# Kernel tuning notes

Measured on AMD Instinct MI355X. Metric: run time of the kernel, lower is better.

The kernel has to match this reference:

```python
import jax, jax.numpy as jnp
import numpy as np

RES = 256      # cubic grid resolution
CH = 16        # feature channels
RR = 8         # reduced_res = ceil(log2(RES))
MASK = 128     # low-frequency mask size
N_PTS = 262144 # query points


def _bilinear(feat, gx, gy):
    """torch.F.grid_sample, bilinear, align_corners=True, zero padding.
    feat: (C,H,W); gx,gy: (N,) in [-1,1] (gx indexes W, gy indexes H).
    Returns (N,C)."""
    H, W = feat.shape[1], feat.shape[2]
    x = (gx + 1.0) * 0.5 * (W - 1)
    y = (gy + 1.0) * 0.5 * (H - 1)
    x0 = jnp.floor(x)
    y0 = jnp.floor(y)
    wx = x - x0
    wy = y - y0
    x0i = jnp.clip(x0.astype(jnp.int32), 0, W - 1)
    x1i = jnp.clip(x0i + 1, 0, W - 1)
    y0i = jnp.clip(y0.astype(jnp.int32), 0, H - 1)
    y1i = jnp.clip(y0i + 1, 0, H - 1)
    v00 = feat[:, y0i, x0i]
    v01 = feat[:, y0i, x1i]
    v10 = feat[:, y1i, x0i]
    v11 = feat[:, y1i, x1i]
    out = (v00 * (1 - wx) * (1 - wy) + v01 * wx * (1 - wy)
           + v10 * (1 - wx) * wy + v11 * wx * wy)  # (C,N)
    return out.T


def _plane(P, mask2d, gx, gy, icoord):
    """One phasor plane: mask -> ifft2 -> grid_sample -> Fourier integration.
    P: (CH*RR, RES, RES, 2); returns (N, CH)."""
    Pc = (P[..., 0] + 1j * P[..., 1]) * mask2d          # (C,H,W) complex
    Pc = jnp.fft.ifft2(Pc)                              # ifft over last 2 axes
    C = P.shape[0]
    # interleave (real, imag) per complex channel, like permute+reshape in torch
    feat = jnp.stack([Pc.real, Pc.imag], axis=1).reshape(2 * C, RES, RES)
    samp = _bilinear(feat, gx, gy).reshape(-1, 2 * CH, RR)  # (N, 2*CH, RR)
    Z = samp[:, :CH] + 1j * samp[:, CH:]                    # (N, CH, RR)
    s = (icoord + 1.0) * 0.5 * (2 ** RR - 1)                # scaled coord
    coef = 2.0 ** jnp.arange(RR) - 1.0                      # (RR,)
    basis = jnp.exp(2j * jnp.pi * s[:, None] * coef / (2 ** RR))  # (N, RR)
    return jnp.einsum('nr,ncr->nc', basis, Z).real


def _forward(Pu, Pv, Pw, inputs):
    mask2d = jnp.zeros((RES, RES), jnp.float32).at[:MASK, :MASK].set(1.0)
    out = (_plane(Pu, mask2d, inputs[:, 1], inputs[:, 2], inputs[:, 0])
           + _plane(Pv, mask2d, inputs[:, 0], inputs[:, 2], inputs[:, 1])
           + _plane(Pw, mask2d, inputs[:, 0], inputs[:, 1], inputs[:, 2]))
    return out  # (N, CH)


def setup_inputs() -> dict:
    key = jax.random.key(0)
    k1, k2, k3, k4 = jax.random.split(key, 4)
    Pu = 0.001 * jax.random.normal(k1, (CH * RR, RES, RES, 2), jnp.float32)
    Pv = 0.001 * jax.random.normal(k2, (CH * RR, RES, RES, 2), jnp.float32)
    Pw = 0.001 * jax.random.normal(k3, (CH * RR, RES, RES, 2), jnp.float32)
    inputs = jax.random.uniform(k4, (N_PTS, 3), jnp.float32, -1.0, 1.0)
    return {"Pu": Pu, "Pv": Pv, "Pw": Pw, "inputs": inputs}


def reference(Pu, Pv, Pw, inputs):
    return _forward(Pu, Pv, Pw, inputs)
```

## Files before the change

### kernel.cpp

```cpp
#include <hip/hip_runtime.h>
#include <hip/hip_bf16.h>
#include <hip/hip_fp16.h>
#include <cmath>


#define NPTS 262144

typedef _Float16 f16x2 __attribute__((ext_vector_type(2)));

__device__ __forceinline__ int brev8(int x) { return (int)(__brev((unsigned)x) >> 24); }

__device__ __forceinline__ int swz(int i) {
    return (i & ~15) | ((i ^ (i >> 4)) & 15);
}

__device__ __forceinline__ unsigned pack_bf16(float2 v) {
    unsigned short a = __builtin_bit_cast(unsigned short, __float2bfloat16(v.x));
    unsigned short b = __builtin_bit_cast(unsigned short, __float2bfloat16(v.y));
    return (unsigned)a | ((unsigned)b << 16);
}
__device__ __forceinline__ float2 unpack_bf16(unsigned u) {
    return make_float2(__uint_as_float(u << 16), __uint_as_float(u & 0xffff0000u));
}

__device__ __forceinline__ float dot2f(unsigned a, unsigned b, float c) {
#if __has_builtin(__builtin_amdgcn_fdot2)
    return __builtin_amdgcn_fdot2(__builtin_bit_cast(f16x2, a),
                                  __builtin_bit_cast(f16x2, b), c, false);
#else
    float d;
    asm("v_dot2_f32_f16 %0, %1, %2, %3" : "=v"(d) : "v"(a), "v"(b), "v"(c));
    return d;
#endif
}

__device__ __forceinline__ void plane_coords(int p, float in0, float in1, float in2,
                                             float& gx, float& gy, float& sc) {
    gx = (p == 0) ? in1 : in0;
    gy = (p == 2) ? in1 : in2;
    sc = (p == 0) ? in0 : ((p == 1) ? in1 : in2);
}

__global__ __launch_bounds__(512) void pass1_kernel(const float* __restrict__ P0,
                                                    const float* __restrict__ P1,
                                                    const float* __restrict__ P2,
                                                    unsigned* __restrict__ X) {
    __shared__ float2 tw[128];
    __shared__ float2 tile[256 * 17];

    int t = threadIdx.x;
    if (t < 128) {
        float s, c;
        sincospif((float)t * (1.0f / 128.0f), &s, &c);
        tw[swz(t)] = make_float2(c, s);
    }
    int plane = blockIdx.y;
    const float* P = (plane == 0) ? P0 : ((plane == 1) ? P1 : P2);
    unsigned* Xp = X + (size_t)plane * 4194304;

    int b  = blockIdx.x;
    int ch = b >> 3;
    int x0 = (b & 7) << 4;
    const float* src = P + (size_t)ch * 131072 + x0 * 2;

    const float scale = 1.0f / 65536.0f;
#pragma unroll
    for (int k = 0; k < 2; k++) {
        int i = t + (k << 9);
        int y = i >> 3;
        int j = i & 7;
        float4 v = *(const float4*)(src + (size_t)y * 512 + (j << 2));
        float2 c0 = make_float2(v.x * scale, v.y * scale);
        float2 c1 = make_float2(v.z * scale, v.w * scale);
        int pos = brev8(y);
        tile[swz(pos) * 17 + 2 * j]           = c0;
        tile[swz(pos + 1) * 17 + 2 * j]       = c0;
        tile[swz(pos) * 17 + 2 * j + 1]       = c1;
        tile[swz(pos + 1) * 17 + 2 * j + 1]   = c1;
    }
    __syncthreads();

    int w = t >> 6, l = t & 63;
    int col = (w << 1) + (l & 1);
    int bb  = l >> 1;
#pragma unroll
    for (int s = 2; s <= 8; s++) {
        int half = 1 << (s - 1);
#pragma unroll
        for (int k = 0; k < 4; k++) {
            int bf = (s == 4) ? ((bb << 2) + k) : (bb + (k << 5));
            int j  = bf & (half - 1);
            int g  = bf >> (s - 1);
            int i0 = (g << s) + j;
            int i1 = i0 + half;
            float2 u = tile[swz(i0) * 17 + col];
            float2 v = tile[swz(i1) * 17 + col];
            float2 wq = tw[swz(j << (8 - s))];
            float2 vt = make_float2(v.x * wq.x - v.y * wq.y, v.x * wq.y + v.y * wq.x);
            tile[swz(i0) * 17 + col] = make_float2(u.x + vt.x, u.y + vt.y);
            tile[swz(i1) * 17 + col] = make_float2(u.x - vt.x, u.y - vt.y);
        }
    }
    __syncthreads();

    unsigned* dst = Xp + (size_t)ch * 32768 + x0;
#pragma unroll
    for (int k = 0; k < 8; k++) {
        int i = t + (k << 9);
        int v = i >> 4;
        int c = i & 15;
        dst[(size_t)v * 128 + c] = pack_bf16(tile[swz(v) * 17 + c]);
    }
}

__global__ __launch_bounds__(1024) void pass2_kernel(const unsigned* __restrict__ X,
                                                     __half* __restrict__ feat) {
    __shared__ float2 tw[128];
    __shared__ float2 rows[16 * 257];

    int t = threadIdx.x;
    if (t < 128) {
        float s, c;
        sincospif((float)t * (1.0f / 128.0f), &s, &c);
        tw[swz(t)] = make_float2(c, s);
    }
    int w = t >> 6;
    int l = t & 63;
    int v   = blockIdx.x & 255;
    int g   = blockIdx.x >> 8;
    int ch0 = g << 4;
    int ch  = ch0 + w;
    int plane = blockIdx.y;
    const unsigned* Xp = X + (size_t)plane * 4194304;
    __half* fp = feat + (size_t)plane * 16777216;

    const uint2* src = (const uint2*)(Xp + ((size_t)ch * 256 + v) * 128);
    uint2 d = src[l];
    float2 c0 = unpack_bf16(d.x);
    float2 c1 = unpack_bf16(d.y);
    float2* row = rows + w * 257;
    int p0 = brev8(2 * l);
    int p1 = brev8(2 * l + 1);
    row[swz(p0)]     = c0;
    row[swz(p0 + 1)] = c0;
    row[swz(p1)]     = c1;
    row[swz(p1 + 1)] = c1;
    __syncthreads();
#pragma unroll
    for (int s = 2; s <= 8; s++) {
        int half = 1 << (s - 1);
#pragma unroll
        for (int k = 0; k < 2; k++) {
            int bf = (s == 4) ? ((l << 1) + k) : (l + (k << 6));
            int j  = bf & (half - 1);
            int gg = bf >> (s - 1);
            int i0 = (gg << s) + j;
            int i1 = i0 + half;
            float2 u  = row[swz(i0)];
            float2 vv = row[swz(i1)];
            float2 wq = tw[swz(j << (8 - s))];
            float2 vt = make_float2(vv.x * wq.x - vv.y * wq.y,
                                    vv.x * wq.y + vv.y * wq.x);
            row[swz(i0)] = make_float2(u.x + vt.x, u.y + vt.y);
            row[swz(i1)] = make_float2(u.x - vt.x, u.y - vt.y);
        }
    }
    __syncthreads();
    __half* dst = fp + (size_t)v * 65536 + (ch0 << 1);
#pragma unroll
    for (int k = 0; k < 8; k++) {
        int f = t + (k << 10);
        int x = f >> 5;
        int j = f & 31;
        float2 cpx = rows[(j >> 1) * 257 + swz(x)];
        float val = (j & 1) ? cpx.y : cpx.x;
        dst[x * 256 + j] = __float2half(val * 16384.0f);
    }
}

__device__ __forceinline__ int tile_key(float gx, float gy) {
    float xf = (gx + 1.0f) * 127.5f;
    float yf = (gy + 1.0f) * 127.5f;
    int x0 = max(0, min((int)floorf(xf), 255));
    int y0 = max(0, min((int)floorf(yf), 255));
    return (y0 & 0xF0) | (x0 >> 4);
}

__global__ __launch_bounds__(1024) void hist_kernel(const float* __restrict__ pts,
                                                    unsigned* __restrict__ hist) {
    __shared__ unsigned hb[256];
    int t = threadIdx.x;
    int p = blockIdx.y;
    int n = (blockIdx.x << 10) + t;
    if (t < 256) hb[t] = 0;
    __syncthreads();
    float in0 = pts[3 * n + 0], in1 = pts[3 * n + 1], in2 = pts[3 * n + 2];
    float gx, gy, sc;
    plane_coords(p, in0, in1, in2, gx, gy, sc);
    atomicAdd(&hb[tile_key(gx, gy)], 1u);
    __syncthreads();
    if (t < 256 && hb[t]) atomicAdd(&hist[(p << 8) + t], hb[t]);
}

__global__ __launch_bounds__(256) void scan_kernel(const unsigned* __restrict__ hist,
                                                   unsigned* __restrict__ cursor) {
    __shared__ unsigned s[256];
    int t = threadIdx.x;
    for (int p = 0; p < 3; p++) {
        unsigned v = hist[(p << 8) + t];
        s[t] = v;
        __syncthreads();
#pragma unroll
        for (int d = 1; d < 256; d <<= 1) {
            unsigned add = (t >= d) ? s[t - d] : 0u;
            __syncthreads();
            s[t] += add;
            __syncthreads();
        }
        cursor[(p << 8) + t] = s[t] - v;
        __syncthreads();
    }
}

__global__ __launch_bounds__(1024) void scatter_kernel(const float* __restrict__ pts,
                                                       unsigned* __restrict__ cursor,
                                                       float4* __restrict__ psort) {
    __shared__ unsigned cnt[256];
    __shared__ unsigned base[256];
    int t = threadIdx.x;
    int p = blockIdx.y;
    int n = (blockIdx.x << 10) + t;
    if (t < 256) cnt[t] = 0;
    __syncthreads();
    float in0 = pts[3 * n + 0], in1 = pts[3 * n + 1], in2 = pts[3 * n + 2];
    float gx, gy, sc;
    plane_coords(p, in0, in1, in2, gx, gy, sc);

    float xf = (gx + 1.0f) * 127.5f;
    float yf = (gy + 1.0f) * 127.5f;
    float x0f = floorf(xf);
    float y0f = floorf(yf);
    float wx = xf - x0f;
    float wy = yf - y0f;
    int x0 = max(0, min((int)x0f, 255));
    int y0 = max(0, min((int)y0f, 255));
    int key = (y0 & 0xF0) | (x0 >> 4);

    unsigned rank = atomicAdd(&cnt[key], 1u);
    __syncthreads();
    if (t < 256 && cnt[t]) base[t] = atomicAdd(&cursor[(p << 8) + t], cnt[t]);
    __syncthreads();

    unsigned pk = ((unsigned)((y0 << 8) + x0) << 8)
                | ((x0 < 255) ? (1u << 24) : 0u)
                | ((y0 < 255) ? (1u << 25) : 0u);
    float sprime = (sc + 1.0f) * 0.99609375f;
    __half2 wh = __floats2half2_rn(wx, wy);
    psort[p * NPTS + base[key] + rank] =
        make_float4(__uint_as_float(pk), __builtin_bit_cast(float, wh),
                    sprime, __int_as_float(n));
}


#define GSTAGE(i)                                                              \
    unsigned pk##i = __float_as_uint(pt##i.x);                                 \
    const ushort* bp##i = fb + (pk##i & 0xFFFFFFu);                            \
    int dx##i = (int)((pk##i >> 16) & 0x100u);                                 \
    int dy##i = (int)((pk##i >> 9) & 0x10000u);                                \
    uint4 e00##i = *(const uint4*)(bp##i);                                     \
    uint4 e01##i = *(const uint4*)(bp##i + dx##i);                             \
    uint4 e10##i = *(const uint4*)(bp##i + dy##i);                             \
    uint4 e11##i = *(const uint4*)(bp##i + dx##i + dy##i);

#define GWORK(i) {                                                             \
    __half2 wh = __builtin_bit_cast(__half2, pt##i.y);                         \
    float wx = __low2float(wh);                                                \
    float wy = __high2float(wh);                                               \
    float a = pt##i.z * coef;                                                  \
    float sn, cs;                                                              \
    sincospif(a, &sn, &cs);                                                    \
    float merged = (q < 16) ? cs : -sn;                                        \
    float partner = __int_as_float(                                            \
        __builtin_amdgcn_ds_swizzle(__float_as_int(merged), 0x041F));          \
    float lo = (l & 1) ? partner : merged;                                     \
    float hi = (l & 1) ? merged : partner;                                     \
    __half2 wp = __floats2half2_rn(lo, hi);                                    \
    unsigned wpi = __builtin_bit_cast(unsigned, wp);                           \
    unsigned w0 = (unsigned)__builtin_amdgcn_ds_swizzle((int)wpi, 0x0010);     \
    unsigned w1 = (unsigned)__builtin_amdgcn_ds_swizzle((int)wpi, 0x0050);     \
    unsigned w2 = (unsigned)__builtin_amdgcn_ds_swizzle((int)wpi, 0x0090);     \
    unsigned w3 = (unsigned)__builtin_amdgcn_ds_swizzle((int)wpi, 0x00D0);     \
    float s00 = dot2f(e00##i.w, w3, dot2f(e00##i.z, w2,                        \
                dot2f(e00##i.y, w1, dot2f(e00##i.x, w0, 0.0f))));              \
    float s01 = dot2f(e01##i.w, w3, dot2f(e01##i.z, w2,                        \
                dot2f(e01##i.y, w1, dot2f(e01##i.x, w0, 0.0f))));              \
    float s10 = dot2f(e10##i.w, w3, dot2f(e10##i.z, w2,                        \
                dot2f(e10##i.y, w1, dot2f(e10##i.x, w0, 0.0f))));              \
    float s11 = dot2f(e11##i.w, w3, dot2f(e11##i.z, w2,                        \
                dot2f(e11##i.y, w1, dot2f(e11##i.x, w0, 0.0f))));              \
    const float INV = 6.103515625e-05f;                                        \
    float wys = wy * INV;                                                      \
    float wyc = INV - wys;                                                     \
    float wxc = 1.0f - wx;                                                     \
    float acc = s00 * (wxc * wyc);                                             \
    acc = fmaf(s01, wx * wyc, acc);                                            \
    acc = fmaf(s10, wxc * wys, acc);                                           \
    acc = fmaf(s11, wx * wys, acc);                                            \
    acc += __int_as_float(                                                     \
        __builtin_amdgcn_ds_swizzle(__float_as_int(acc), 0x401F));             \
    if (q < 16) {                                                              \
        int n = __float_as_int(pt##i.w);                                       \
        atomicAdd(&out[((size_t)n << 4) + q], acc);                            \
    } }

__global__ __launch_bounds__(256) void gather_kernel(const ushort* __restrict__ feat,
                                                     const float4* __restrict__ psort,
                                                     float* __restrict__ out) {
    int t = threadIdx.x;
    int w = t >> 6;
    int l = t & 63;
    int h = l >> 5;
    int q = l & 31;
    int p = blockIdx.y;
    const ushort* fb = feat + (size_t)p * 16777216 + (q << 3);

    int b  = blockIdx.x;
    int lb = ((b & 7) << 10) | (b >> 3);
    const float4* ps = psort + p * NPTS + (lb << 5) + (w << 1) + h;

    float4 pt0 = ps[0];
    float4 pt1 = ps[8];
    float4 pt2 = ps[16];
    float4 pt3 = ps[24];

    float coef = (float)((1 << (q & 7)) - 1);

    GSTAGE(0)
    GSTAGE(1)
    GWORK(0)
    GSTAGE(2)
    GWORK(1)
    GSTAGE(3)
    GWORK(2)
    GWORK(3)
}

__global__ __launch_bounds__(256) void combine_kernel(const float4* __restrict__ pa,
                                                      float4* __restrict__ out) {
    int i = (blockIdx.x << 8) + threadIdx.x;
    float4 a = pa[i];
    float4 b = pa[i + 1048576];
    float4 c = pa[i + 2097152];
    out[i] = make_float4(a.x + b.x + c.x, a.y + b.y + c.y,
                         a.z + b.z + c.z, a.w + b.w + c.w);
}

extern "C" void kernel_launch(void* const* d_in, const int* in_sizes, int n_in,
                              void* d_out, int out_size, void* d_ws, size_t ws_size,
                              hipStream_t stream) {
    const float* P0  = (const float*)d_in[0];
    const float* P1  = (const float*)d_in[1];
    const float* P2  = (const float*)d_in[2];
    const float* pts = (const float*)d_in[3];
    float* out = (float*)d_out;
    char* ws = (char*)d_ws;

    __half*   feat   = (__half*)ws;
    unsigned* X      = (unsigned*)(ws + 100663296u);
    float4*   psort  = (float4*)(ws + 201326592u);
    unsigned* hist   = (unsigned*)(ws + 213909504u);
    unsigned* cursor = (unsigned*)(ws + 213912576u);

    hipMemsetAsync(hist, 0, 3072, stream);
    hipMemsetAsync(out, 0, (size_t)NPTS * 64, stream);

    dim3 g1(1024, 3);
    pass1_kernel<<<g1, 512, 0, stream>>>(P0, P1, P2, X);
    dim3 g2(2048, 3);
    pass2_kernel<<<g2, 1024, 0, stream>>>(X, feat);

    dim3 gs(256, 3);
    hist_kernel<<<gs, 1024, 0, stream>>>(pts, hist);
    scan_kernel<<<1, 256, 0, stream>>>(hist, cursor);
    scatter_kernel<<<gs, 1024, 0, stream>>>(pts, cursor, psort);

    dim3 gg(8192, 3);
    gather_kernel<<<gg, 256, 0, stream>>>((const ushort*)feat, psort, out);
}
```

Baseline: 346.8 us.

## Precompute Fourier basis weights in scatter pass and split scan per plane

The scatter kernel now computes the eight cos/sin basis terms per point with one sincospi and angle-doubling recurrences, packs them as fp16 and writes them to a new per-point weight buffer. The gather kernel loads these 32-byte weights instead of evaluating sincospi per lane and shuffling the results across lanes with swizzles. The scan kernel is also split into three blocks, one per plane. The trade is extra global traffic (about 25 MB written and read) and some recurrence rounding error, in exchange for less transcendental and cross-lane work in the gather.

```diff
diff --git a/kernel.cpp b/kernel.cpp
--- a/kernel.cpp
+++ b/kernel.cpp
@@ -21,6 +21,10 @@
 }
 __device__ __forceinline__ float2 unpack_bf16(unsigned u) {
     return make_float2(__uint_as_float(u << 16), __uint_as_float(u & 0xffff0000u));
+}
+__device__ __forceinline__ unsigned pack_h2(float a, float b) {
+    __half2 h = __floats2half2_rn(a, b);
+    return __builtin_bit_cast(unsigned, h);
 }
 
 __device__ __forceinline__ float dot2f(unsigned a, unsigned b, float c) {
@@ -206,25 +210,24 @@
                                                    unsigned* __restrict__ cursor) {
     __shared__ unsigned s[256];
     int t = threadIdx.x;
-    for (int p = 0; p < 3; p++) {
-        unsigned v = hist[(p << 8) + t];
-        s[t] = v;
+    int p = blockIdx.y;
+    unsigned v = hist[(p << 8) + t];
+    s[t] = v;
+    __syncthreads();
+#pragma unroll
+    for (int d = 1; d < 256; d <<= 1) {
+        unsigned add = (t >= d) ? s[t - d] : 0u;
         __syncthreads();
-#pragma unroll
-        for (int d = 1; d < 256; d <<= 1) {
-            unsigned add = (t >= d) ? s[t - d] : 0u;
-            __syncthreads();
-            s[t] += add;
-            __syncthreads();
-        }
-        cursor[(p << 8) + t] = s[t] - v;
+        s[t] += add;
         __syncthreads();
     }
+    cursor[(p << 8) + t] = s[t] - v;
 }
 
 __global__ __launch_bounds__(1024) void scatter_kernel(const float* __restrict__ pts,
                                                        unsigned* __restrict__ cursor,
-                                                       float4* __restrict__ psort) {
+                                                       float4* __restrict__ psort,
+                                                       uint4* __restrict__ pweight) {
     __shared__ unsigned cnt[256];
     __shared__ unsigned base[256];
     int t = threadIdx.x;
@@ -254,11 +257,34 @@
     unsigned pk = ((unsigned)((y0 << 8) + x0) << 8)
                 | ((x0 < 255) ? (1u << 24) : 0u)
                 | ((y0 < 255) ? (1u << 25) : 0u);
-    float sprime = (sc + 1.0f) * 0.99609375f;
+    float sp = (sc + 1.0f) * 0.99609375f;
     __half2 wh = __floats2half2_rn(wx, wy);
-    psort[p * NPTS + base[key] + rank] =
+    int o = base[key] + rank;
+    psort[p * NPTS + o] =
         make_float4(__uint_as_float(pk), __builtin_bit_cast(float, wh),
-                    sprime, __int_as_float(n));
+                    0.0f, __int_as_float(n));
+
+    float c1, s1;
+    sincospif(sp, &s1, &c1);
+    float cc = c1, ss = s1;
+    float cA[8], sA[8];
+    cA[0] = 1.0f; sA[0] = 0.0f;
+    cA[1] = c1;  sA[1] = s1;
+#pragma unroll
+    for (int r = 2; r < 8; r++) {
+        float c2 = cc * cc - ss * ss;
+        float s2 = 2.0f * cc * ss;
+        cc = c2 * c1 - s2 * s1;
+        ss = c2 * s1 + s2 * c1;
+        cA[r] = cc; sA[r] = ss;
+    }
+    uint4 cb = make_uint4(pack_h2(cA[0], cA[1]), pack_h2(cA[2], cA[3]),
+                          pack_h2(cA[4], cA[5]), pack_h2(cA[6], cA[7]));
+    uint4 sb = make_uint4(pack_h2(-sA[0], -sA[1]), pack_h2(-sA[2], -sA[3]),
+                          pack_h2(-sA[4], -sA[5]), pack_h2(-sA[6], -sA[7]));
+    size_t wo = ((size_t)p * NPTS + o) << 1;
+    pweight[wo]     = cb;
+    pweight[wo + 1] = sb;
 }
 
 
@@ -276,28 +302,14 @@
     __half2 wh = __builtin_bit_cast(__half2, pt##i.y);                         \
     float wx = __low2float(wh);                                                \
     float wy = __high2float(wh);                                               \
-    float a = pt##i.z * coef;                                                  \
-    float sn, cs;                                                              \
-    sincospif(a, &sn, &cs);                                                    \
-    float merged = (q < 16) ? cs : -sn;                                        \
-    float partner = __int_as_float(                                            \
-        __builtin_amdgcn_ds_swizzle(__float_as_int(merged), 0x041F));          \
-    float lo = (l & 1) ? partner : merged;                                     \
-    float hi = (l & 1) ? merged : partner;                                     \
-    __half2 wp = __floats2half2_rn(lo, hi);                                    \
-    unsigned wpi = __builtin_bit_cast(unsigned, wp);                           \
-    unsigned w0 = (unsigned)__builtin_amdgcn_ds_swizzle((int)wpi, 0x0010);     \
-    unsigned w1 = (unsigned)__builtin_amdgcn_ds_swizzle((int)wpi, 0x0050);     \
-    unsigned w2 = (unsigned)__builtin_amdgcn_ds_swizzle((int)wpi, 0x0090);     \
-    unsigned w3 = (unsigned)__builtin_amdgcn_ds_swizzle((int)wpi, 0x00D0);     \
-    float s00 = dot2f(e00##i.w, w3, dot2f(e00##i.z, w2,                        \
-                dot2f(e00##i.y, w1, dot2f(e00##i.x, w0, 0.0f))));              \
-    float s01 = dot2f(e01##i.w, w3, dot2f(e01##i.z, w2,                        \
-                dot2f(e01##i.y, w1, dot2f(e01##i.x, w0, 0.0f))));              \
-    float s10 = dot2f(e10##i.w, w3, dot2f(e10##i.z, w2,                        \
-                dot2f(e10##i.y, w1, dot2f(e10##i.x, w0, 0.0f))));              \
-    float s11 = dot2f(e11##i.w, w3, dot2f(e11##i.z, w2,                        \
-                dot2f(e11##i.y, w1, dot2f(e11##i.x, w0, 0.0f))));              \
+    float s00 = dot2f(e00##i.w, ww##i.w, dot2f(e00##i.z, ww##i.z,              \
+                dot2f(e00##i.y, ww##i.y, dot2f(e00##i.x, ww##i.x, 0.0f))));    \
+    float s01 = dot2f(e01##i.w, ww##i.w, dot2f(e01##i.z, ww##i.z,              \
+                dot2f(e01##i.y, ww##i.y, dot2f(e01##i.x, ww##i.x, 0.0f))));    \
+    float s10 = dot2f(e10##i.w, ww##i.w, dot2f(e10##i.z, ww##i.z,              \
+                dot2f(e10##i.y, ww##i.y, dot2f(e10##i.x, ww##i.x, 0.0f))));    \
+    float s11 = dot2f(e11##i.w, ww##i.w, dot2f(e11##i.z, ww##i.z,              \
+                dot2f(e11##i.y, ww##i.y, dot2f(e11##i.x, ww##i.x, 0.0f))));    \
     const float INV = 6.103515625e-05f;                                        \
     float wys = wy * INV;                                                      \
     float wyc = INV - wys;                                                     \
@@ -315,6 +327,7 @@
 
 __global__ __launch_bounds__(256) void gather_kernel(const ushort* __restrict__ feat,
                                                      const float4* __restrict__ psort,
+                                                     const uint4* __restrict__ pweight,
                                                      float* __restrict__ out) {
     int t = threadIdx.x;
     int w = t >> 6;
@@ -326,14 +339,18 @@
 
     int b  = blockIdx.x;
     int lb = ((b & 7) << 10) | (b >> 3);
-    const float4* ps = psort + p * NPTS + (lb << 5) + (w << 1) + h;
+    int idx0 = (lb << 5) + (w << 1) + h;
+    const float4* ps = psort + p * NPTS + idx0;
+    const uint4* pw = pweight + (((size_t)p * NPTS + idx0) << 1) + (q >> 4);
 
     float4 pt0 = ps[0];
     float4 pt1 = ps[8];
     float4 pt2 = ps[16];
     float4 pt3 = ps[24];
-
-    float coef = (float)((1 << (q & 7)) - 1);
+    uint4 ww0 = pw[0];
+    uint4 ww1 = pw[16];
+    uint4 ww2 = pw[32];
+    uint4 ww3 = pw[48];
 
     GSTAGE(0)
     GSTAGE(1)
@@ -343,16 +360,6 @@
     GSTAGE(3)
     GWORK(2)
     GWORK(3)
-}
-
-__global__ __launch_bounds__(256) void combine_kernel(const float4* __restrict__ pa,
-                                                      float4* __restrict__ out) {
-    int i = (blockIdx.x << 8) + threadIdx.x;
-    float4 a = pa[i];
-    float4 b = pa[i + 1048576];
-    float4 c = pa[i + 2097152];
-    out[i] = make_float4(a.x + b.x + c.x, a.y + b.y + c.y,
-                         a.z + b.z + c.z, a.w + b.w + c.w);
 }
 
 extern "C" void kernel_launch(void* const* d_in, const int* in_sizes, int n_in,
@@ -365,11 +372,12 @@
     float* out = (float*)d_out;
     char* ws = (char*)d_ws;
 
-    __half*   feat   = (__half*)ws;
-    unsigned* X      = (unsigned*)(ws + 100663296u);
-    float4*   psort  = (float4*)(ws + 201326592u);
-    unsigned* hist   = (unsigned*)(ws + 213909504u);
-    unsigned* cursor = (unsigned*)(ws + 213912576u);
+    __half*   feat    = (__half*)ws;
+    unsigned* X       = (unsigned*)(ws + 100663296u);
+    uint4*    pweight = (uint4*)(ws + 150994944u);
+    float4*   psort   = (float4*)(ws + 201326592u);
+    unsigned* hist    = (unsigned*)(ws + 213909504u);
+    unsigned* cursor  = (unsigned*)(ws + 213912576u);
 
     hipMemsetAsync(hist, 0, 3072, stream);
     hipMemsetAsync(out, 0, (size_t)NPTS * 64, stream);
@@ -381,9 +389,9 @@
 
     dim3 gs(256, 3);
     hist_kernel<<<gs, 1024, 0, stream>>>(pts, hist);
-    scan_kernel<<<1, 256, 0, stream>>>(hist, cursor);
-    scatter_kernel<<<gs, 1024, 0, stream>>>(pts, cursor, psort);
+    scan_kernel<<<dim3(1, 3), 256, 0, stream>>>(hist, cursor);
+    scatter_kernel<<<gs, 1024, 0, stream>>>(pts, cursor, psort, pweight);
 
     dim3 gg(8192, 3);
-    gather_kernel<<<gg, 256, 0, stream>>>((const ushort*)feat, psort, out);
-}
+    gather_kernel<<<gg, 256, 0, stream>>>((const ushort*)feat, psort, pweight, out);
+}
```

Measured after the change: 377.9 us. 9.0% more time.
